# Performance work log

Hardware: AMD Instinct MI355X
Metric: run time of the kernel (lower is better)

## Reference

```python
import jax, jax.numpy as jnp
import numpy as np

B, N = 2, 512
D_NODE, D_EDGE, D_HID, H = 128, 64, 128, 8
DH = D_HID // H  # per-head dim = 16
SCALE = 1.0 / (D_HID ** 0.5)  # note: scale uses full d_hid as in source


def setup_inputs() -> dict:
    key = jax.random.key(0)
    k1, k2, k3, k4 = jax.random.split(key, 4)
    node_features = jax.random.normal(k1, (B, N, D_NODE), dtype=jnp.float32)
    edge_features = jax.random.normal(k2, (B, N, N, D_EDGE), dtype=jnp.float32)
    mask = jnp.ones((B, N, N), dtype=bool)
    # Linear weights (stored as (in, out); math identical to torch x @ W.T)
    W_node = jax.random.normal(k3, (D_NODE, 3 * D_HID), dtype=jnp.float32) / np.sqrt(D_NODE)
    W_edge = jax.random.normal(k4, (D_EDGE, 3 * D_HID), dtype=jnp.float32) / np.sqrt(D_EDGE)
    return {"node_features": node_features, "edge_features": edge_features,
            "mask": mask, "W_node": W_node, "W_edge": W_edge}


def _split_heads_node(x):
    # (b, n, h*c) -> (b, h, n, c)
    b, n, hc = x.shape
    return x.reshape(b, n, H, hc // H).transpose(0, 2, 1, 3)


def _split_heads_edge(x):
    # (b, n, m, h*c) -> (b, h, n, m, c)
    b, n, m, hc = x.shape
    return x.reshape(b, n, m, H, hc // H).transpose(0, 3, 1, 2, 4)


def reference(node_features, edge_features, mask, W_node, W_edge):
    # node qkv: (b, n, 3*d_hid) -> (b, h, n, 3*dh) -> chunk
    qkv_n = _split_heads_node(node_features @ W_node)
    q_node, k_node, v_node = jnp.split(qkv_n, 3, axis=-1)  # each (b,h,n,dh)
    # edge qkv: (b, n, n, 3*d_hid) -> (b, h, n, n, 3*dh) -> chunk
    qkv_e = _split_heads_edge(edge_features @ W_edge)
    q_edge, k_edge, v_edge = jnp.split(qkv_e, 3, axis=-1)  # each (b,h,n,n,dh)

    q = q_node[:, :, :, None, :] + q_edge   # (b,h,i,j,dh)
    k = k_node[:, :, None, :, :] + k_edge   # (b,h,i,j,dh)
    v = v_node[:, :, None, :, :] + v_edge   # (b,h,i,j,dh)

    dots = SCALE * jnp.einsum('bhijd,bhijd->bhij', q, k)
    attn = jax.nn.softmax(dots, axis=-1)
    out = jnp.einsum('bhij,bhijd->bhid', attn, v)  # (b,h,n,dh)
    # (b,h,n,dh) -> (b,n,h*dh)
    b, h, n, dh = out.shape
    return out.transpose(0, 2, 1, 3).reshape(b, n, h * dh)
```

## Files before the change

### kernel.cpp

```cpp
#include <hip/hip_runtime.h>
#include <hip/hip_bf16.h>

#define NN 512
#define OC 384
#define S2F 0.12751694f

typedef __attribute__((ext_vector_type(8))) short short8;
typedef __attribute__((ext_vector_type(4))) float f32x4;

#define LD4(p) (*reinterpret_cast<const f32x4*>(p))

__device__ __forceinline__ unsigned short f2bf(float x) {
    unsigned u = __builtin_bit_cast(unsigned, x);
    u = (u + 0x7fffu + ((u >> 16) & 1u)) >> 16;
    return (unsigned short)u;
}

__device__ __forceinline__ ushort4 cvt4(f32x4 a) {
    union { ushort4 u4; __hip_bfloat162 h[2]; } r;
    r.h[0] = __float22bfloat162_rn(make_float2(a[0], a[1]));
    r.h[1] = __float22bfloat162_rn(make_float2(a[2], a[3]));
    return r.u4;
}

__global__ __launch_bounds__(256) void prep0_kernel(
    const float* __restrict__ Wn, const float* __restrict__ We,
    const float* __restrict__ node,
    unsigned short* __restrict__ WtN, unsigned short* __restrict__ WtE,
    unsigned short* __restrict__ nodeBf)
{
    int idx = blockIdx.x * 256 + threadIdx.x;
    if (idx < 24576) {
        int o = idx >> 6, k = idx & 63;
        WtE[idx] = f2bf(We[k * OC + o]);
    } else if (idx < 24576 + 49152) {
        int id = idx - 24576;
        int o = id >> 7, k = id & 127;
        WtN[id] = f2bf(Wn[k * OC + o]);
    } else {
        int id = idx - 73728;
        nodeBf[id] = f2bf(node[id]);
    }
}

__global__ __launch_bounds__(256) void prep1_kernel(
    const unsigned short* __restrict__ nodeBf,
    const unsigned short* __restrict__ WtN,
    float* __restrict__ qnF,
    float* __restrict__ nodeKV)
{
    const int t = threadIdx.x;
    const int w = t >> 6;
    const int lane = t & 63;
    const int lj = lane & 15;
    const int quad = lane >> 4;
    const int nbase = blockIdx.x * 32;

    short8 bfr[2][4];
#pragma unroll
    for (int nt = 0; nt < 2; ++nt)
#pragma unroll
        for (int ks = 0; ks < 4; ++ks)
            bfr[nt][ks] = *reinterpret_cast<const short8*>(
                nodeBf + (size_t)(nbase + nt * 16 + lj) * 128 + ks * 32 + quad * 8);

#pragma unroll
    for (int m = 0; m < 6; ++m) {
        int ot = (6 * w + m) * 16;
        short8 afr[4];
#pragma unroll
        for (int ks = 0; ks < 4; ++ks)
            afr[ks] = *reinterpret_cast<const short8*>(
                WtN + (size_t)(ot + lj) * 128 + ks * 32 + quad * 8);
#pragma unroll
        for (int nt = 0; nt < 2; ++nt) {
            f32x4 acc = {0.f, 0.f, 0.f, 0.f};
#pragma unroll
            for (int ks = 0; ks < 4; ++ks)
                acc = __builtin_amdgcn_mfma_f32_16x16x32_bf16(afr[ks], bfr[nt][ks], acc, 0, 0, 0);
            int n = nbase + nt * 16 + lj;
            int bb = n >> 9, ii = n & 511;
#pragma unroll
            for (int r = 0; r < 4; ++r) {
                int o = ot + quad * 4 + r;
                int h = o / 48, rem = o - h * 48;
                if (rem < 16) {
                    qnF[((size_t)(bb * 8 + h) * NN + ii) * 16 + rem] = acc[r];
                } else {
                    int d = (rem - 16) & 15;
                    int kv = (rem >= 32) ? 1 : 0;
                    size_t slot = ((((size_t)(bb * 8 + h) * 4 + (d >> 2)) * 2 + kv) * NN + ii) * 4 + (d & 3);
                    nodeKV[slot] = acc[r];
                }
            }
        }
    }
}

__global__ __launch_bounds__(512, 3) void rt_attn_main(
    const float* __restrict__ edge,
    const float* __restrict__ qnF,
    const float* __restrict__ nodeKV,
    const unsigned short* __restrict__ WtE,
    float* __restrict__ out)
{
    __shared__ unsigned short sE[2][64 * 72];
    const int bi = blockIdx.x;
    const int b = bi >> 9;
    const int i = bi & 511;
    const int t = threadIdx.x;
    const int h = t >> 6;
    const int lane = t & 63;
    const int lj = lane & 15;
    const int quad = lane >> 4;

    const int sj0 = t >> 4;
    const int sj1 = sj0 + 32;
    const int sc = (t & 15) * 4;

    const float* eBase = edge + (size_t)bi * NN * 64;
    f32x4 pf0, pf1;
    pf0 = LD4(eBase + (size_t)sj0 * 64 + sc);
    pf1 = LD4(eBase + (size_t)sj1 * 64 + sc);

    short8 afr[3][2];
#pragma unroll
    for (int T = 0; T < 3; ++T)
#pragma unroll
        for (int sec = 0; sec < 2; ++sec)
            afr[T][sec] = *reinterpret_cast<const short8*>(
                WtE + (size_t)(h * 48 + T * 16 + lj) * 64 + sec * 32 + quad * 8);

    const f32x4 qn = LD4(qnF + ((size_t)(b * 8 + h) * NN + i) * 16 + quad * 4);

    const float* kvB = nodeKV + ((size_t)(b * 8 + h) * 4 + quad) * (2 * NN * 4) + (size_t)lj * 4;

    f32x4 ka[2][4], va[2][4];
#pragma unroll
    for (int jn = 0; jn < 4; ++jn) {
        const float* kvp = kvB + (size_t)(jn * 16) * 4;
        ka[0][jn] = LD4(kvp);
        va[0][jn] = LD4(kvp + NN * 4);
    }

    float l = 0.f;
    float oa[4] = {0.f, 0.f, 0.f, 0.f};

    {
        *reinterpret_cast<ushort4*>(&sE[0][sj0 * 72 + sc]) = cvt4(pf0);
        *reinterpret_cast<ushort4*>(&sE[0][sj1 * 72 + sc]) = cvt4(pf1);
    }
    __syncthreads();

#pragma unroll
    for (int tt = 0; tt < 8; ++tt) {
        const int cur = tt & 1;
        if (tt < 7) {
            const float* nb = eBase + (size_t)(tt + 1) * 4096;
            pf0 = LD4(nb + (size_t)sj0 * 64 + sc);
            pf1 = LD4(nb + (size_t)sj1 * 64 + sc);
        }
        if (tt < 7) {
#pragma unroll
            for (int jn = 0; jn < 4; ++jn) {
                const float* kvp = kvB + (size_t)((tt + 1) * 64 + jn * 16) * 4;
                ka[cur ^ 1][jn] = LD4(kvp);
                va[cur ^ 1][jn] = LD4(kvp + NN * 4);
            }
        }
        float dp[4];
        f32x4 fvv[4];
#pragma unroll
        for (int jn = 0; jn < 4; ++jn) {
            const int jrow = jn * 16 + lj;
            short8 b0 = *reinterpret_cast<const short8*>(&sE[cur][jrow * 72 + quad * 8]);
            short8 b1 = *reinterpret_cast<const short8*>(&sE[cur][jrow * 72 + 32 + quad * 8]);
            f32x4 fq = qn;
            fq = __builtin_amdgcn_mfma_f32_16x16x32_bf16(afr[0][0], b0, fq, 0, 0, 0);
            fq = __builtin_amdgcn_mfma_f32_16x16x32_bf16(afr[0][1], b1, fq, 0, 0, 0);
            f32x4 fk = ka[cur][jn];
            fk = __builtin_amdgcn_mfma_f32_16x16x32_bf16(afr[1][0], b0, fk, 0, 0, 0);
            fk = __builtin_amdgcn_mfma_f32_16x16x32_bf16(afr[1][1], b1, fk, 0, 0, 0);
            f32x4 fv = va[cur][jn];
            fv = __builtin_amdgcn_mfma_f32_16x16x32_bf16(afr[2][0], b0, fv, 0, 0, 0);
            fv = __builtin_amdgcn_mfma_f32_16x16x32_bf16(afr[2][1], b1, fv, 0, 0, 0);
            fvv[jn] = fv;
            float d0 = fq[0] * fk[0];
            d0 = fmaf(fq[1], fk[1], d0);
            d0 = fmaf(fq[2], fk[2], d0);
            d0 = fmaf(fq[3], fk[3], d0);
            dp[jn] = d0;
        }
        float t16[4], t32[4], wg[4];
#pragma unroll
        for (int jn = 0; jn < 4; ++jn) t16[jn] = __shfl_xor(dp[jn], 16);
#pragma unroll
        for (int jn = 0; jn < 4; ++jn) dp[jn] += t16[jn];
#pragma unroll
        for (int jn = 0; jn < 4; ++jn) t32[jn] = __shfl_xor(dp[jn], 32);
#pragma unroll
        for (int jn = 0; jn < 4; ++jn) {
            wg[jn] = exp2f((dp[jn] + t32[jn]) * S2F);
            l += wg[jn];
        }
#pragma unroll
        for (int jn = 0; jn < 4; ++jn)
#pragma unroll
            for (int r = 0; r < 4; ++r)
                oa[r] = fmaf(wg[jn], fvv[jn][r], oa[r]);
        if (tt < 7) {
            *reinterpret_cast<ushort4*>(&sE[cur ^ 1][sj0 * 72 + sc]) = cvt4(pf0);
            *reinterpret_cast<ushort4*>(&sE[cur ^ 1][sj1 * 72 + sc]) = cvt4(pf1);
            __syncthreads();
        }
    }

#pragma unroll
    for (int off = 1; off <= 8; off <<= 1) {
        l += __shfl_xor(l, off);
#pragma unroll
        for (int r = 0; r < 4; ++r) oa[r] += __shfl_xor(oa[r], off);
    }
    if (lj == 0) {
        float inv = 1.0f / l;
        f32x4 o4;
#pragma unroll
        for (int r = 0; r < 4; ++r) o4[r] = oa[r] * inv;
        *reinterpret_cast<f32x4*>(out + (size_t)bi * 128 + h * 16 + quad * 4) = o4;
    }
}

extern "C" void kernel_launch(void* const* d_in, const int* in_sizes, int n_in,
                              void* d_out, int out_size, void* d_ws, size_t ws_size,
                              hipStream_t stream) {
    const float* node = (const float*)d_in[0];
    const float* edge = (const float*)d_in[1];
    const float* Wn = (const float*)d_in[3];
    const float* We = (const float*)d_in[4];
    float* out = (float*)d_out;

    char* ws = (char*)d_ws;
    float* qnF = (float*)ws;
    float* nodeKV = (float*)(ws + 524288);
    unsigned short* WtE = (unsigned short*)(ws + 1572864);
    unsigned short* WtN = (unsigned short*)(ws + 1622016);
    unsigned short* nodeBf = (unsigned short*)(ws + 1720320);

    prep0_kernel<<<800, 256, 0, stream>>>(Wn, We, node, WtN, WtE, nodeBf);
    prep1_kernel<<<32, 256, 0, stream>>>(nodeBf, WtN, qnF, nodeKV);
    rt_attn_main<<<2 * NN, 512, 0, stream>>>(edge, qnF, nodeKV, WtE, out);
}
```

Before: 225.7 us.

## Split attention over j-tiles with partial sums and a combine kernel

Each main-kernel block now handles four query rows i and one 64-wide j tile instead of one i over all 512 j. Per-tile numerators and softmax denominators go to workspace, and a new combine kernel sums them and divides. Node K/V for the tile is loaded once and reused across the four rows, and the grid grows from 1024 to 2048 blocks. In exchange it adds an extra launch and partial-result traffic, and it lowers the occupancy hint from 3 to 2 blocks per CU.

Result: slower. 232.8 us (+3.2%).

```diff
diff --git a/kernel.cpp b/kernel.cpp
--- a/kernel.cpp
+++ b/kernel.cpp
@@ -97,17 +97,20 @@
     }
 }
 
-__global__ __launch_bounds__(512, 3) void rt_attn_main(
+__global__ __launch_bounds__(512, 2) void rt_attn_main(
     const float* __restrict__ edge,
     const float* __restrict__ qnF,
     const float* __restrict__ nodeKV,
     const unsigned short* __restrict__ WtE,
-    float* __restrict__ out)
+    float* __restrict__ oaP,
+    float* __restrict__ lP)
 {
     __shared__ unsigned short sE[2][64 * 72];
-    const int bi = blockIdx.x;
-    const int b = bi >> 9;
-    const int i = bi & 511;
+    const int blk = blockIdx.x;
+    const int jt = blk & 7;
+    const int ic = (blk >> 3) & 127;
+    const int b  = blk >> 10;
+    const int i0 = ic * 4;
     const int t = threadIdx.x;
     const int h = t >> 6;
     const int lane = t & 63;
@@ -118,10 +121,9 @@
     const int sj1 = sj0 + 32;
     const int sc = (t & 15) * 4;
 
-    const float* eBase = edge + (size_t)bi * NN * 64;
-    f32x4 pf0, pf1;
-    pf0 = LD4(eBase + (size_t)sj0 * 64 + sc);
-    pf1 = LD4(eBase + (size_t)sj1 * 64 + sc);
+    const float* eB = edge + ((size_t)(b * NN + i0) * NN + jt * 64) * 64;
+    f32x4 pf0 = LD4(eB + (size_t)sj0 * 64 + sc);
+    f32x4 pf1 = LD4(eB + (size_t)sj1 * 64 + sc);
 
     short8 afr[3][2];
 #pragma unroll
@@ -131,20 +133,17 @@
             afr[T][sec] = *reinterpret_cast<const short8*>(
                 WtE + (size_t)(h * 48 + T * 16 + lj) * 64 + sec * 32 + quad * 8);
 
-    const f32x4 qn = LD4(qnF + ((size_t)(b * 8 + h) * NN + i) * 16 + quad * 4);
-
     const float* kvB = nodeKV + ((size_t)(b * 8 + h) * 4 + quad) * (2 * NN * 4) + (size_t)lj * 4;
-
-    f32x4 ka[2][4], va[2][4];
+    f32x4 ka[4], va[4];
 #pragma unroll
     for (int jn = 0; jn < 4; ++jn) {
-        const float* kvp = kvB + (size_t)(jn * 16) * 4;
-        ka[0][jn] = LD4(kvp);
-        va[0][jn] = LD4(kvp + NN * 4);
-    }
-
-    float l = 0.f;
-    float oa[4] = {0.f, 0.f, 0.f, 0.f};
+        const float* kvp = kvB + (size_t)(jt * 64 + jn * 16) * 4;
+        ka[jn] = LD4(kvp);
+        va[jn] = LD4(kvp + NN * 4);
+    }
+
+    const float* qB = qnF + ((size_t)(b * 8 + h) * NN + i0) * 16 + quad * 4;
+    f32x4 qnC = LD4(qB);
 
     {
         *reinterpret_cast<ushort4*>(&sE[0][sj0 * 72 + sc]) = cvt4(pf0);
@@ -153,20 +152,14 @@
     __syncthreads();
 
 #pragma unroll
-    for (int tt = 0; tt < 8; ++tt) {
-        const int cur = tt & 1;
-        if (tt < 7) {
-            const float* nb = eBase + (size_t)(tt + 1) * 4096;
+    for (int ii = 0; ii < 4; ++ii) {
+        const int cur = ii & 1;
+        f32x4 qnN;
+        if (ii < 3) {
+            const float* nb = eB + (size_t)(ii + 1) * (NN * 64);
             pf0 = LD4(nb + (size_t)sj0 * 64 + sc);
             pf1 = LD4(nb + (size_t)sj1 * 64 + sc);
-        }
-        if (tt < 7) {
-#pragma unroll
-            for (int jn = 0; jn < 4; ++jn) {
-                const float* kvp = kvB + (size_t)((tt + 1) * 64 + jn * 16) * 4;
-                ka[cur ^ 1][jn] = LD4(kvp);
-                va[cur ^ 1][jn] = LD4(kvp + NN * 4);
-            }
+            qnN = LD4(qB + (ii + 1) * 16);
         }
         float dp[4];
         f32x4 fvv[4];
@@ -175,13 +168,13 @@
             const int jrow = jn * 16 + lj;
             short8 b0 = *reinterpret_cast<const short8*>(&sE[cur][jrow * 72 + quad * 8]);
             short8 b1 = *reinterpret_cast<const short8*>(&sE[cur][jrow * 72 + 32 + quad * 8]);
-            f32x4 fq = qn;
+            f32x4 fq = qnC;
             fq = __builtin_amdgcn_mfma_f32_16x16x32_bf16(afr[0][0], b0, fq, 0, 0, 0);
             fq = __builtin_amdgcn_mfma_f32_16x16x32_bf16(afr[0][1], b1, fq, 0, 0, 0);
-            f32x4 fk = ka[cur][jn];
+            f32x4 fk = ka[jn];
             fk = __builtin_amdgcn_mfma_f32_16x16x32_bf16(afr[1][0], b0, fk, 0, 0, 0);
             fk = __builtin_amdgcn_mfma_f32_16x16x32_bf16(afr[1][1], b1, fk, 0, 0, 0);
-            f32x4 fv = va[cur][jn];
+            f32x4 fv = va[jn];
             fv = __builtin_amdgcn_mfma_f32_16x16x32_bf16(afr[2][0], b0, fv, 0, 0, 0);
             fv = __builtin_amdgcn_mfma_f32_16x16x32_bf16(afr[2][1], b1, fv, 0, 0, 0);
             fvv[jn] = fv;
@@ -192,6 +185,7 @@
             dp[jn] = d0;
         }
         float t16[4], t32[4], wg[4];
+        float l = 0.f;
 #pragma unroll
         for (int jn = 0; jn < 4; ++jn) t16[jn] = __shfl_xor(dp[jn], 16);
 #pragma unroll
@@ -203,31 +197,53 @@
             wg[jn] = exp2f((dp[jn] + t32[jn]) * S2F);
             l += wg[jn];
         }
+        float oa[4] = {0.f, 0.f, 0.f, 0.f};
 #pragma unroll
         for (int jn = 0; jn < 4; ++jn)
 #pragma unroll
             for (int r = 0; r < 4; ++r)
                 oa[r] = fmaf(wg[jn], fvv[jn][r], oa[r]);
-        if (tt < 7) {
+#pragma unroll
+        for (int off = 1; off <= 8; off <<= 1) {
+            l += __shfl_xor(l, off);
+#pragma unroll
+            for (int r = 0; r < 4; ++r) oa[r] += __shfl_xor(oa[r], off);
+        }
+        if (lj == 0) {
+            size_t pbase = ((size_t)(b * 8 + h) * 8 + jt) * NN + (i0 + ii);
+            f32x4 o4;
+#pragma unroll
+            for (int r = 0; r < 4; ++r) o4[r] = oa[r];
+            *reinterpret_cast<f32x4*>(oaP + pbase * 16 + quad * 4) = o4;
+            if (quad == 0) lP[pbase] = l;
+        }
+        if (ii < 3) {
             *reinterpret_cast<ushort4*>(&sE[cur ^ 1][sj0 * 72 + sc]) = cvt4(pf0);
             *reinterpret_cast<ushort4*>(&sE[cur ^ 1][sj1 * 72 + sc]) = cvt4(pf1);
             __syncthreads();
-        }
-    }
-
-#pragma unroll
-    for (int off = 1; off <= 8; off <<= 1) {
-        l += __shfl_xor(l, off);
-#pragma unroll
-        for (int r = 0; r < 4; ++r) oa[r] += __shfl_xor(oa[r], off);
-    }
-    if (lj == 0) {
-        float inv = 1.0f / l;
-        f32x4 o4;
-#pragma unroll
-        for (int r = 0; r < 4; ++r) o4[r] = oa[r] * inv;
-        *reinterpret_cast<f32x4*>(out + (size_t)bi * 128 + h * 16 + quad * 4) = o4;
-    }
+            qnC = qnN;
+        }
+    }
+}
+
+__global__ __launch_bounds__(256) void combine_kernel(
+    const float* __restrict__ oaP,
+    const float* __restrict__ lP,
+    float* __restrict__ out)
+{
+    int tid = blockIdx.x * 256 + threadIdx.x;
+    int d = tid & 15;
+    int i = (tid >> 4) & 511;
+    int h = (tid >> 13) & 7;
+    int b = tid >> 16;
+    float num = 0.f, den = 0.f;
+#pragma unroll
+    for (int jt = 0; jt < 8; ++jt) {
+        size_t pb = ((size_t)(b * 8 + h) * 8 + jt) * NN + i;
+        num += oaP[pb * 16 + d];
+        den += lP[pb];
+    }
+    out[((size_t)b * NN + i) * 128 + h * 16 + d] = num / den;
 }
 
 extern "C" void kernel_launch(void* const* d_in, const int* in_sizes, int n_in,
@@ -245,8 +261,11 @@
     unsigned short* WtE = (unsigned short*)(ws + 1572864);
     unsigned short* WtN = (unsigned short*)(ws + 1622016);
     unsigned short* nodeBf = (unsigned short*)(ws + 1720320);
+    float* oaP = (float*)(ws + 2097152);
+    float* lP  = (float*)(ws + 6291456);
 
     prep0_kernel<<<800, 256, 0, stream>>>(Wn, We, node, WtN, WtE, nodeBf);
     prep1_kernel<<<32, 256, 0, stream>>>(nodeBf, WtN, qnF, nodeKV);
-    rt_attn_main<<<2 * NN, 512, 0, stream>>>(edge, qnF, nodeKV, WtE, out);
-}
+    rt_attn_main<<<2 * 128 * 8, 512, 0, stream>>>(edge, qnF, nodeKV, WtE, oaP, lP);
+    combine_kernel<<<512, 256, 0, stream>>>(oaP, lP, out);
+}
```
